# Kernel tuning notes

Hardware: AMD Instinct MI355X
Metric: run time of the kernel (lower is better)

The kernel has to match this reference:

```python
import jax, jax.numpy as jnp
import numpy as np

B, T, V, H, C = 512, 512, 64, 128, 4


def setup_inputs() -> dict:
    key = jax.random.key(0)
    ks = jax.random.split(key, 32)
    s = 0.05  # weight scale
    inp = {
        'x': jax.random.normal(ks[0], (B, T, V), jnp.float32),
        'd': jax.random.uniform(ks[1], (B, T, 1), jnp.float32),
        'm1': (jax.random.uniform(ks[2], (B, T, V)) < 0.5).astype(jnp.float32),
        'h0_1': 0.1 * jax.random.normal(ks[3], (B, H), jnp.float32),
        'h0_2': 0.1 * jax.random.normal(ks[4], (B, H), jnp.float32),
        'h0_3': 0.1 * jax.random.normal(ks[5], (B, H), jnp.float32),
        'W_ih1': s * jax.random.normal(ks[6], (3 * H, V), jnp.float32),
        'W_hh1': s * jax.random.normal(ks[7], (3 * H, H), jnp.float32),
        'b_ih1': jnp.zeros((3 * H,), jnp.float32),
        'b_hh1': jnp.zeros((3 * H,), jnp.float32),
        'W_ih2': s * jax.random.normal(ks[8], (3 * H, H), jnp.float32),
        'W_hh2': s * jax.random.normal(ks[9], (3 * H, H), jnp.float32),
        'b_ih2': jnp.zeros((3 * H,), jnp.float32),
        'b_hh2': jnp.zeros((3 * H,), jnp.float32),
        'W_ih3': s * jax.random.normal(ks[10], (3 * H, H), jnp.float32),
        'W_hh3': s * jax.random.normal(ks[11], (3 * H, H), jnp.float32),
        'b_ih3': jnp.zeros((3 * H,), jnp.float32),
        'b_hh3': jnp.zeros((3 * H,), jnp.float32),
        'W_out': s * jax.random.normal(ks[12], (C, H), jnp.float32),
        'b_out': jax.random.uniform(ks[13], (C,), jnp.float32),
        'W_dx': s * jax.random.normal(ks[14], (V, 1), jnp.float32),
        'b_dx': jax.random.uniform(ks[15], (V,), jnp.float32),
        'W_dh': s * jax.random.normal(ks[16], (H, 1), jnp.float32),
        'b_dh': jax.random.uniform(ks[17], (H,), jnp.float32),
    }
    return inp


def _gru_cell(xt, h, Wih, Whh, bih, bhh):
    # torch.nn.GRUCell math
    gi = xt @ Wih.T + bih          # [B, 3H]
    gh = h @ Whh.T + bhh           # [B, 3H]
    ir, iz, inn = jnp.split(gi, 3, axis=1)
    hr, hz, hn = jnp.split(gh, 3, axis=1)
    r = jax.nn.sigmoid(ir + hr)
    z = jax.nn.sigmoid(iz + hz)
    n = jnp.tanh(inn + r * hn)
    return (1.0 - z) * n + z * h


def reference(x, d, m1, h0_1, h0_2, h0_3,
              W_ih1, W_hh1, b_ih1, b_hh1,
              W_ih2, W_hh2, b_ih2, b_hh2,
              W_ih3, W_hh3, b_ih3, b_hh3,
              W_out, b_out, W_dx, b_dx, W_dh, b_dh):
    x0 = x[:, 0, :]  # first observation used for imputation

    def head(h):
        return jax.nn.softmax(h @ W_out.T + b_out, axis=1)

    # t = 0: no decay, raw input
    h1 = _gru_cell(x0, h0_1, W_ih1, W_hh1, b_ih1, b_hh1)
    h2 = _gru_cell(h1, h0_2, W_ih2, W_hh2, b_ih2, b_hh2)
    h3 = _gru_cell(h2, h0_3, W_ih3, W_hh3, b_ih3, b_hh3)
    y0 = head(h3)

    # time-major scan inputs for t = 1..T-1
    xs = (jnp.swapaxes(x[:, 1:, :], 0, 1),   # x_t
          jnp.swapaxes(x[:, :-1, :], 0, 1),  # x_{t-1}
          jnp.swapaxes(m1[:, 1:, :], 0, 1),  # m_t
          jnp.swapaxes(d[:, 1:, :], 0, 1))   # d_t [T-1, B, 1]

    def step(carry, inp):
        h1, h2, h3 = carry
        xt, xp, mt, dt = inp
        gamma_h = jnp.exp(-jax.nn.relu(dt @ W_dh.T + b_dh))  # [B, H]
        h1 = h1 * gamma_h
        h2 = h2 * gamma_h
        h3 = h3 * gamma_h
        gamma_x = jnp.exp(-jax.nn.relu(dt @ W_dx.T + b_dx))  # [B, V]
        x1 = (xp * gamma_x + (1.0 - gamma_x) * x0) * (1.0 - mt) + mt * xt
        h1 = _gru_cell(x1, h1, W_ih1, W_hh1, b_ih1, b_hh1)
        h2 = _gru_cell(h1, h2, W_ih2, W_hh2, b_ih2, b_hh2)
        h3 = _gru_cell(h2, h3, W_ih3, W_hh3, b_ih3, b_hh3)
        return (h1, h2, h3), head(h3)

    _, ys = jax.lax.scan(step, (h1, h2, h3), xs)  # [T-1, B, C]
    Y = jnp.concatenate([y0[None], ys], axis=0)    # [T, B, C]
    return jnp.swapaxes(Y, 0, 1)                   # [B, T, C]
```

## Files before the change

kernel.cpp:

```cpp
#include <hip/hip_runtime.h>

#define TT 512
#define VV 64
#define RING 16

typedef _Float16 f16;
typedef f16 f16x8 __attribute__((ext_vector_type(8)));
typedef f16 f16x4 __attribute__((ext_vector_type(4)));
typedef float f32x4v __attribute__((ext_vector_type(4)));
typedef unsigned long long u64;
typedef unsigned u32;

typedef __attribute__((address_space(1))) unsigned gu32;
typedef __attribute__((address_space(1))) unsigned long long gu64;

#define MFMA(A_,B_,C_) __builtin_amdgcn_mfma_f32_16x16x32_f16((A_),(B_),(C_),0,0,0)
#define AT_LD32(p)   __hip_atomic_load((gu32*)(void*)(p), __ATOMIC_RELAXED, __HIP_MEMORY_SCOPE_AGENT)
#define AT_ST32(p,v) __hip_atomic_store((gu32*)(void*)(p),(v), __ATOMIC_RELAXED, __HIP_MEMORY_SCOPE_AGENT)
#define AT_LD64(p)   __hip_atomic_load((gu64*)(void*)(p), __ATOMIC_RELAXED, __HIP_MEMORY_SCOPE_AGENT)
#define AT_ST64(p,v) __hip_atomic_store((gu64*)(void*)(p),(v), __ATOMIC_RELAXED, __HIP_MEMORY_SCOPE_AGENT)

__device__ __forceinline__ void barrier_lds(){ asm volatile("s_waitcnt lgkmcnt(0)\n\ts_barrier" ::: "memory"); }
__device__ __forceinline__ void wait_vm0(){ asm volatile("s_waitcnt vmcnt(0)" ::: "memory"); }
__device__ __forceinline__ float4 ld4(const float* p){ return *(const float4*)p; }

__device__ __forceinline__ f16x8 ldA8(const float* p){
  f16x8 a;
  #pragma unroll
  for (int j = 0; j < 8; ++j) a[j] = (f16)p[j];
  return a;
}

__device__ __forceinline__ int fragOff16(int d0, int b){
  const int kt = d0 >> 5, qq = (d0 >> 3) & 3, j0 = d0 & 7;
  return (kt*64 + qq*16 + b)*8 + j0;
}

__device__ __forceinline__ void fragW_lds(f16x8* buf, int d0, int b, const float* h4){
  f16x4 v;
  #pragma unroll
  for (int e = 0; e < 4; ++e) v[e] = (f16)h4[e];
  *(f16x4*)((f16*)buf + fragOff16(d0, b)) = v;
}

__device__ __forceinline__ void pubFrag(char* slot, int d0, int b, const float* h4){
  union { f16x4 v; u64 u; } uu;
  #pragma unroll
  for (int e = 0; e < 4; ++e) uu.v[e] = (f16)h4[e];
  AT_ST64((u64*)(slot + fragOff16(d0, b)*2), uu.u);
}

__device__ __forceinline__ f16x8 impFrag(const char* slot, int kt, int lane){
  union { u64 u[2]; f16x8 v; } vv;
  const u64* p = (const u64*)(slot + (kt*64 + lane)*16);
  vv.u[0] = AT_LD64((u64*)p);
  vv.u[1] = AT_LD64((u64*)(p + 1));
  return vv.v;
}

__device__ __forceinline__ void spin_ge(u32* f, u32 val){
  if ((threadIdx.x & 63) == 0){
    u32 g = 0;
    while (AT_LD32(f) < val && ++g < (1u << 20)) {}
  }
  asm volatile("" ::: "memory");
}

__device__ __forceinline__ void gates_upd2(const f32x4v& C0, const f32x4v& C1,
                                           const f32x4v& Ci2, const f32x4v& Ch2,
                                           const float* bR, const float* bZ,
                                           const float* bI, const float* bH,
                                           float* hp){
  #pragma unroll
  for (int e = 0; e < 4; ++e){
    float rr = 1.f/(1.f + __expf(-(C0[e] + bR[e])));
    float zz = 1.f/(1.f + __expf(-(C1[e] + bZ[e])));
    float nv = Ci2[e] + bI[e] + rr*(Ch2[e] + bH[e]);
    float nn = 1.f - 2.f/(1.f + __expf(2.f*nv));
    hp[e] = (1.f - zz)*nn + zz*hp[e];
  }
}

__global__ void k_init(u32* wsf){
  const int i = blockIdx.x*256 + threadIdx.x;
  if (i < 4096) AT_ST32(wsf + i, 0u);
}

__launch_bounds__(512, 1)
__global__ void k_pipe(const float* __restrict__ x,   const float* __restrict__ dd,
                       const float* __restrict__ m1,
                       const float* __restrict__ h01, const float* __restrict__ h02,
                       const float* __restrict__ h03,
                       const float* __restrict__ Wih1, const float* __restrict__ Whh1,
                       const float* __restrict__ bih1, const float* __restrict__ bhh1,
                       const float* __restrict__ Wih2, const float* __restrict__ Whh2,
                       const float* __restrict__ bih2, const float* __restrict__ bhh2,
                       const float* __restrict__ Wih3, const float* __restrict__ Whh3,
                       const float* __restrict__ bih3, const float* __restrict__ bhh3,
                       const float* __restrict__ Wout, const float* __restrict__ bout,
                       const float* __restrict__ Wdx,  const float* __restrict__ bdx,
                       const float* __restrict__ Wdh,  const float* __restrict__ bdh,
                       float* __restrict__ y, u32* __restrict__ wsf, char* __restrict__ wsd)
{
  __shared__ f16x8 sW[8*12*64];
  __shared__ f16x8 sFrag[2][256];
  __shared__ f16x8 sX1[2][128];
  __shared__ f16x8 sHead[2][256];

  const int tid = threadIdx.x, wid = tid >> 6, lane = tid & 63;
  const int q = lane >> 4, r = lane & 15;
  const int blk = blockIdx.x, role = blk >> 5, grp = blk & 31, b0 = grp << 4;

  u32* const FL  = wsf;
  u32* const ACK = wsf + 1024;
  u32* const fl0 = FL  + grp*16;
  u32* const ak0 = ACK + grp*16;
  u32* const fl1 = FL  + (32+grp)*16;
  u32* const ak1 = ACK + (32+grp)*16;
  char* const ring0 = wsd + (size_t)grp*RING*4096;
  char* const ring1 = wsd + (size_t)(32+grp)*RING*4096;

  const int dG = wid*16 + 4*q;
  const int wbase = wid*12;

  const float* bihX = (role == 0) ? bih1 : (role == 1) ? bih2 : bih3;
  const float* bhhX = (role == 0) ? bhh1 : (role == 1) ? bhh2 : bhh3;
  const float* h0X  = (role == 0) ? h01  : (role == 1) ? h02  : h03;

  float bR[4], bZ[4], bI[4], bH[4], hS[4], WdhL[4], bdhL[4];
  #pragma unroll
  for (int e = 0; e < 4; ++e){
    const int d = dG + e;
    bR[e] = bihX[d] + bhhX[d];
    bZ[e] = bihX[128+d] + bhhX[128+d];
    bI[e] = bihX[256+d];
    bH[e] = bhhX[256+d];
    WdhL[e] = Wdh[d]; bdhL[e] = bdh[d];
  }
  { float4 a = ld4(h0X + (size_t)(b0+r)*128 + dG); hS[0]=a.x; hS[1]=a.y; hS[2]=a.z; hS[3]=a.w; }
  float dhC = 0.f, dhN = dd[(size_t)(b0+r)*TT + 1];

  if (role == 0){
    f16x8 Ai[3][2];
    #pragma unroll
    for (int g = 0; g < 3; ++g){
      const int mrow = (g*8 + wid)*16 + r;
      #pragma unroll
      for (int kt = 0; kt < 2; ++kt) Ai[g][kt] = ldA8(Wih1 + mrow*64 + kt*32 + q*8);
      #pragma unroll
      for (int kt = 0; kt < 4; ++kt)
        sW[(wbase + g*4 + kt)*64 + lane] = ldA8(Whh1 + mrow*128 + kt*32 + q*8);
    }
    const int bx = (wid & 3)*4 + q, v0 = 4*r;
    float Wdx4[4] = {0,0,0,0}, bdx4[4] = {0,0,0,0};
    float4 xC = {0,0,0,0}, x0v = {0,0,0,0}, xN = {0,0,0,0}, mN = {0,0,0,0};
    float4 xP = {0,0,0,0}, mC = {0,0,0,0};
    float dxC = 0.f, dxN = 0.f;
    if (wid < 4){
      #pragma unroll
      for (int e = 0; e < 4; ++e){ Wdx4[e] = Wdx[v0+e]; bdx4[e] = bdx[v0+e]; }
      xC  = ld4(x + ((size_t)(b0+bx)*TT + 0)*VV + v0);
      x0v = xC;
      xN  = ld4(x  + ((size_t)(b0+bx)*TT + 1)*VV + v0);
      mN  = ld4(m1 + ((size_t)(b0+bx)*TT + 1)*VV + v0);
      dxN = dd[(size_t)(b0+bx)*TT + 1];
      xP = xC; mC = mN; dxC = dxN;
    }
    __syncthreads();

    for (int t = 0; t < TT; ++t){
      const int par = t & 1;
      if ((t & 3) == 0 && t >= 16) spin_ge(ak0, (u32)(t-13));
      if (wid < 4){
        float xi[4];
        if (t == 0){ xi[0]=xC.x; xi[1]=xC.y; xi[2]=xC.z; xi[3]=xC.w; }
        else {
          const float* xc = (const float*)&xC; const float* xp = (const float*)&xP;
          const float* x0e = (const float*)&x0v; const float* me = (const float*)&mC;
          #pragma unroll
          for (int e = 0; e < 4; ++e){
            float gx = __expf(-fmaxf(dxC*Wdx4[e] + bdx4[e], 0.f));
            xi[e] = (xp[e]*gx + (1.f-gx)*x0e[e])*(1.f-me[e]) + me[e]*xc[e];
          }
        }
        fragW_lds(&sX1[par][0], v0, bx, xi);
      }
      if (t >= 1){
        #pragma unroll
        for (int e = 0; e < 4; ++e)
          hS[e] *= __expf(-fmaxf(dhC*WdhL[e] + bdhL[e], 0.f));
      }
      fragW_lds(&sFrag[par][0], dG, r, hS);
      barrier_lds();
      f16x8 bx1[2], bh4[4];
      #pragma unroll
      for (int kt = 0; kt < 2; ++kt) bx1[kt] = sX1[par][kt*64 + lane];
      #pragma unroll
      for (int kt = 0; kt < 4; ++kt) bh4[kt] = sFrag[par][kt*64 + lane];
      f32x4v C0 = {0,0,0,0}, C1 = {0,0,0,0}, Ci2 = {0,0,0,0}, Ch2 = {0,0,0,0};
      #pragma unroll
      for (int kt = 0; kt < 4; ++kt) C0  = MFMA(sW[(wbase + 0*4 + kt)*64 + lane], bh4[kt], C0);
      #pragma unroll
      for (int kt = 0; kt < 4; ++kt) C1  = MFMA(sW[(wbase + 1*4 + kt)*64 + lane], bh4[kt], C1);
      #pragma unroll
      for (int kt = 0; kt < 4; ++kt) Ch2 = MFMA(sW[(wbase + 2*4 + kt)*64 + lane], bh4[kt], Ch2);
      #pragma unroll
      for (int kt = 0; kt < 2; ++kt) C0  = MFMA(Ai[0][kt], bx1[kt], C0);
      #pragma unroll
      for (int kt = 0; kt < 2; ++kt) C1  = MFMA(Ai[1][kt], bx1[kt], C1);
      #pragma unroll
      for (int kt = 0; kt < 2; ++kt) Ci2 = MFMA(Ai[2][kt], bx1[kt], Ci2);
      gates_upd2(C0, C1, Ci2, Ch2, bR, bZ, bI, bH, hS);
      pubFrag(ring0 + (size_t)(t & (RING-1))*4096, dG, r, hS);
      if ((t & 3) == 3){
        wait_vm0();
        barrier_lds();
        if (tid == 0) AT_ST32(fl0, (u32)(t+1));
      }
      dhC = dhN;
      const int tp = (t+2 < TT) ? (t+2) : (TT-1);
      dhN = dd[(size_t)(b0+r)*TT + tp];
      if (wid < 4){
        xP = xC; xC = xN; mC = mN; dxC = dxN;
        xN  = ld4(x  + ((size_t)(b0+bx)*TT + tp)*VV + v0);
        mN  = ld4(m1 + ((size_t)(b0+bx)*TT + tp)*VV + v0);
        dxN = dd[(size_t)(b0+bx)*TT + tp];
      }
    }
    return;
  }

  if (role == 1){
    f16x8 Ah[3][4];
    #pragma unroll
    for (int g = 0; g < 3; ++g){
      const int mrow = (g*8 + wid)*16 + r;
      #pragma unroll
      for (int kt = 0; kt < 4; ++kt){
        sW[(wbase + g*4 + kt)*64 + lane] = ldA8(Wih2 + mrow*128 + kt*32 + q*8);
        Ah[g][kt] = ldA8(Whh2 + mrow*128 + kt*32 + q*8);
      }
    }
    __syncthreads();

    spin_ge(fl0, 8u);
    f16x8 bi[4];
    #pragma unroll
    for (int kt = 0; kt < 4; ++kt) bi[kt] = impFrag(ring0, kt, lane);

    for (int t = 0; t < TT; ++t){
      const int par = t & 1;
      if ((t & 3) == 0 && t >= 16) spin_ge(ak1, (u32)(t-13));
      if (t >= 1){
        #pragma unroll
        for (int e = 0; e < 4; ++e)
          hS[e] *= __expf(-fmaxf(dhC*WdhL[e] + bdhL[e], 0.f));
      }
      fragW_lds(&sFrag[par][0], dG, r, hS);
      barrier_lds();
      if (tid == 0) AT_ST32(ak0, (u32)t);
      f16x8 bh4[4];
      #pragma unroll
      for (int kt = 0; kt < 4; ++kt) bh4[kt] = sFrag[par][kt*64 + lane];
      f32x4v C0 = {0,0,0,0}, C1 = {0,0,0,0}, Ci2 = {0,0,0,0}, Ch2 = {0,0,0,0};
      #pragma unroll
      for (int kt = 0; kt < 4; ++kt) C0  = MFMA(Ah[0][kt], bh4[kt], C0);
      #pragma unroll
      for (int kt = 0; kt < 4; ++kt) C1  = MFMA(Ah[1][kt], bh4[kt], C1);
      #pragma unroll
      for (int kt = 0; kt < 4; ++kt) Ch2 = MFMA(Ah[2][kt], bh4[kt], Ch2);
      #pragma unroll
      for (int kt = 0; kt < 4; ++kt) C0  = MFMA(sW[(wbase + 0*4 + kt)*64 + lane], bi[kt], C0);
      #pragma unroll
      for (int kt = 0; kt < 4; ++kt) C1  = MFMA(sW[(wbase + 1*4 + kt)*64 + lane], bi[kt], C1);
      #pragma unroll
      for (int kt = 0; kt < 4; ++kt) Ci2 = MFMA(sW[(wbase + 2*4 + kt)*64 + lane], bi[kt], Ci2);
      if (t + 1 < TT){
        const char* sIn = ring0 + (size_t)((t+1) & (RING-1))*4096;
        #pragma unroll
        for (int kt = 0; kt < 4; ++kt) bi[kt] = impFrag(sIn, kt, lane);
      }
      gates_upd2(C0, C1, Ci2, Ch2, bR, bZ, bI, bH, hS);
      pubFrag(ring1 + (size_t)(t & (RING-1))*4096, dG, r, hS);
      if ((t & 3) == 3){
        wait_vm0();
        barrier_lds();
        if (tid == 0) AT_ST32(fl1, (u32)(t+1));
        if (t < TT-1) spin_ge(fl0, (u32)(t+7 <= TT ? t+7 : TT));
      }
      dhC = dhN;
      const int tp = (t+2 < TT) ? (t+2) : (TT-1);
      dhN = dd[(size_t)(b0+r)*TT + tp];
    }
    return;
  }

  {
    f16x8 Ah[3][4];
    #pragma unroll
    for (int g = 0; g < 3; ++g){
      const int mrow = (g*8 + wid)*16 + r;
      #pragma unroll
      for (int kt = 0; kt < 4; ++kt){
        sW[(wbase + g*4 + kt)*64 + lane] = ldA8(Wih3 + mrow*128 + kt*32 + q*8);
        Ah[g][kt] = ldA8(Whh3 + mrow*128 + kt*32 + q*8);
      }
    }
    f16x8 aO[4]; float bo4[4] = {0,0,0,0};
    if (wid == 4){
      #pragma unroll
      for (int kt = 0; kt < 4; ++kt){
        f16x8 a;
        #pragma unroll
        for (int j = 0; j < 8; ++j)
          a[j] = (r < 4) ? (f16)Wout[r*128 + kt*32 + q*8 + j] : (f16)0.f;
        aO[kt] = a;
      }
      #pragma unroll
      for (int e = 0; e < 4; ++e) bo4[e] = bout[e];
    }
    __syncthreads();

    spin_ge(fl1, 8u);
    f16x8 bi[4];
    #pragma unroll
    for (int kt = 0; kt < 4; ++kt) bi[kt] = impFrag(ring1, kt, lane);

    for (int s = 0; s <= TT; ++s){
      const int par = s & 1;
      fragW_lds(&sHead[par][0], dG, r, hS);
      if (s < TT){
        if (s >= 1){
          #pragma unroll
          for (int e = 0; e < 4; ++e)
            hS[e] *= __expf(-fmaxf(dhC*WdhL[e] + bdhL[e], 0.f));
        }
        fragW_lds(&sFrag[par][0], dG, r, hS);
      }
      barrier_lds();
      if (s < TT && tid == 0) AT_ST32(ak1, (u32)s);
      if (s < TT){
        f16x8 bh4[4];
        #pragma unroll
        for (int kt = 0; kt < 4; ++kt) bh4[kt] = sFrag[par][kt*64 + lane];
        f32x4v C0 = {0,0,0,0}, C1 = {0,0,0,0}, Ci2 = {0,0,0,0}, Ch2 = {0,0,0,0};
        #pragma unroll
        for (int kt = 0; kt < 4; ++kt) C0  = MFMA(Ah[0][kt], bh4[kt], C0);
        #pragma unroll
        for (int kt = 0; kt < 4; ++kt) C1  = MFMA(Ah[1][kt], bh4[kt], C1);
        #pragma unroll
        for (int kt = 0; kt < 4; ++kt) Ch2 = MFMA(Ah[2][kt], bh4[kt], Ch2);
        #pragma unroll
        for (int kt = 0; kt < 4; ++kt) C0  = MFMA(sW[(wbase + 0*4 + kt)*64 + lane], bi[kt], C0);
        #pragma unroll
        for (int kt = 0; kt < 4; ++kt) C1  = MFMA(sW[(wbase + 1*4 + kt)*64 + lane], bi[kt], C1);
        #pragma unroll
        for (int kt = 0; kt < 4; ++kt) Ci2 = MFMA(sW[(wbase + 2*4 + kt)*64 + lane], bi[kt], Ci2);
        if (s + 1 < TT){
          const char* sIn = ring1 + (size_t)((s+1) & (RING-1))*4096;
          #pragma unroll
          for (int kt = 0; kt < 4; ++kt) bi[kt] = impFrag(sIn, kt, lane);
        }
        gates_upd2(C0, C1, Ci2, Ch2, bR, bZ, bI, bH, hS);
      }
      if (s >= 1 && wid == 4){
        f32x4v cl = {0.f,0.f,0.f,0.f};
        #pragma unroll
        for (int kt = 0; kt < 4; ++kt) cl = MFMA(aO[kt], sHead[par][kt*64 + lane], cl);
        if (lane < 16){
          float l0 = cl[0]+bo4[0], l1 = cl[1]+bo4[1], l2 = cl[2]+bo4[2], l3 = cl[3]+bo4[3];
          float mx = fmaxf(fmaxf(l0,l1), fmaxf(l2,l3));
          float e0 = __expf(l0-mx), e1 = __expf(l1-mx), e2 = __expf(l2-mx), e3 = __expf(l3-mx);
          float inv = 1.f/(e0+e1+e2+e3);
          float4 o; o.x = e0*inv; o.y = e1*inv; o.z = e2*inv; o.w = e3*inv;
          *(float4*)(y + ((size_t)(b0+lane)*TT + (s-1))*4) = o;
        }
      }
      if ((s & 3) == 3 && s < TT-1) spin_ge(fl1, (u32)(s+7 <= TT ? s+7 : TT));
      dhC = dhN;
      const int tp = (s+2 < TT) ? (s+2) : (TT-1);
      dhN = dd[(size_t)(b0+r)*TT + tp];
    }
  }
}

extern "C" void kernel_launch(void* const* d_in, const int* in_sizes, int n_in,
                              void* d_out, int out_size, void* d_ws, size_t ws_size,
                              hipStream_t stream) {
  (void)in_sizes; (void)n_in; (void)out_size; (void)ws_size;
  u32*  wsf = (u32*)d_ws;
  char* wsd = (char*)d_ws + 16384;
  k_init<<<dim3(16), dim3(256), 0, stream>>>(wsf);
  k_pipe<<<dim3(96), dim3(512), 0, stream>>>(
      (const float*)d_in[0],  (const float*)d_in[1],  (const float*)d_in[2],
      (const float*)d_in[3],  (const float*)d_in[4],  (const float*)d_in[5],
      (const float*)d_in[6],  (const float*)d_in[7],  (const float*)d_in[8],  (const float*)d_in[9],
      (const float*)d_in[10], (const float*)d_in[11], (const float*)d_in[12], (const float*)d_in[13],
      (const float*)d_in[14], (const float*)d_in[15], (const float*)d_in[16], (const float*)d_in[17],
      (const float*)d_in[18], (const float*)d_in[19],
      (const float*)d_in[20], (const float*)d_in[21],
      (const float*)d_in[22], (const float*)d_in[23],
      (float*)d_out, wsf, wsd);
}
```

Measured before the change: 1.266 ms.

## Process 32 batch rows per block with two MFMA halves, halving grid

Each workgroup now handles 32 batch rows instead of 16, running the per-step GRU matmuls twice (two 16-column halves) with the LDS-resident weights reused across both. The grid shrinks from 96 to 48 blocks, and ring slots double to 8 KB per step. The aim is to amortize weight loading, barriers and flag synchronisation over more work per block. The cost is roughly twice the serial per-step latency inside each block, and fewer CUs are in use.

New measurement: 2.016 ms. +59.3%, slower.

```diff
diff --git a/kernel.cpp b/kernel.cpp
--- a/kernel.cpp
+++ b/kernel.cpp
@@ -3,6 +3,8 @@
 #define TT 512
 #define VV 64
 #define RING 16
+#define NG 16
+#define SLOTB 8192
 
 typedef _Float16 f16;
 typedef f16 f16x8 __attribute__((ext_vector_type(8)));
@@ -103,22 +105,22 @@
                        float* __restrict__ y, u32* __restrict__ wsf, char* __restrict__ wsd)
 {
   __shared__ f16x8 sW[8*12*64];
-  __shared__ f16x8 sFrag[2][256];
-  __shared__ f16x8 sX1[2][128];
-  __shared__ f16x8 sHead[2][256];
+  __shared__ f16x8 sFrag[2][512];
+  __shared__ f16x8 sXH[2][256];
+  __shared__ f16x8 sHead[2][512];
 
   const int tid = threadIdx.x, wid = tid >> 6, lane = tid & 63;
   const int q = lane >> 4, r = lane & 15;
-  const int blk = blockIdx.x, role = blk >> 5, grp = blk & 31, b0 = grp << 4;
+  const int blk = blockIdx.x, role = blk >> 4, grp = blk & (NG-1), b0 = grp << 5;
 
   u32* const FL  = wsf;
   u32* const ACK = wsf + 1024;
   u32* const fl0 = FL  + grp*16;
   u32* const ak0 = ACK + grp*16;
-  u32* const fl1 = FL  + (32+grp)*16;
-  u32* const ak1 = ACK + (32+grp)*16;
-  char* const ring0 = wsd + (size_t)grp*RING*4096;
-  char* const ring1 = wsd + (size_t)(32+grp)*RING*4096;
+  u32* const fl1 = FL  + (NG+grp)*16;
+  u32* const ak1 = ACK + (NG+grp)*16;
+  char* const ring0 = wsd + (size_t)grp*RING*SLOTB;
+  char* const ring1 = wsd + (size_t)(NG+grp)*RING*SLOTB;
 
   const int dG = wid*16 + 4*q;
   const int wbase = wid*12;
@@ -127,7 +129,8 @@
   const float* bhhX = (role == 0) ? bhh1 : (role == 1) ? bhh2 : bhh3;
   const float* h0X  = (role == 0) ? h01  : (role == 1) ? h02  : h03;
 
-  float bR[4], bZ[4], bI[4], bH[4], hS[4], WdhL[4], bdhL[4];
+  float bR[4], bZ[4], bI[4], bH[4], WdhL[4], bdhL[4];
+  float hS[2][4];
   #pragma unroll
   for (int e = 0; e < 4; ++e){
     const int d = dG + e;
@@ -137,8 +140,14 @@
     bH[e] = bhhX[256+d];
     WdhL[e] = Wdh[d]; bdhL[e] = bdh[d];
   }
-  { float4 a = ld4(h0X + (size_t)(b0+r)*128 + dG); hS[0]=a.x; hS[1]=a.y; hS[2]=a.z; hS[3]=a.w; }
-  float dhC = 0.f, dhN = dd[(size_t)(b0+r)*TT + 1];
+  { float4 a = ld4(h0X + (size_t)(b0+r)*128 + dG);
+    hS[0][0]=a.x; hS[0][1]=a.y; hS[0][2]=a.z; hS[0][3]=a.w; }
+  { float4 a = ld4(h0X + (size_t)(b0+16+r)*128 + dG);
+    hS[1][0]=a.x; hS[1][1]=a.y; hS[1][2]=a.z; hS[1][3]=a.w; }
+  float dhC[2], dhN[2];
+  dhC[0] = dhC[1] = 0.f;
+  dhN[0] = dd[(size_t)(b0+r)*TT + 1];
+  dhN[1] = dd[(size_t)(b0+16+r)*TT + 1];
 
   if (role == 0){
     f16x8 Ai[3][2];
@@ -151,81 +160,83 @@
       for (int kt = 0; kt < 4; ++kt)
         sW[(wbase + g*4 + kt)*64 + lane] = ldA8(Whh1 + mrow*128 + kt*32 + q*8);
     }
-    const int bx = (wid & 3)*4 + q, v0 = 4*r;
-    float Wdx4[4] = {0,0,0,0}, bdx4[4] = {0,0,0,0};
-    float4 xC = {0,0,0,0}, x0v = {0,0,0,0}, xN = {0,0,0,0}, mN = {0,0,0,0};
-    float4 xP = {0,0,0,0}, mC = {0,0,0,0};
-    float dxC = 0.f, dxN = 0.f;
-    if (wid < 4){
-      #pragma unroll
-      for (int e = 0; e < 4; ++e){ Wdx4[e] = Wdx[v0+e]; bdx4[e] = bdx[v0+e]; }
-      xC  = ld4(x + ((size_t)(b0+bx)*TT + 0)*VV + v0);
-      x0v = xC;
-      xN  = ld4(x  + ((size_t)(b0+bx)*TT + 1)*VV + v0);
-      mN  = ld4(m1 + ((size_t)(b0+bx)*TT + 1)*VV + v0);
-      dxN = dd[(size_t)(b0+bx)*TT + 1];
-      xP = xC; mC = mN; dxC = dxN;
-    }
+    const int bx = wid*4 + q, v0 = 4*r;
+    const int xh = bx >> 4, xc = bx & 15;
+    float Wdx4[4], bdx4[4];
+    #pragma unroll
+    for (int e = 0; e < 4; ++e){ Wdx4[e] = Wdx[v0+e]; bdx4[e] = bdx[v0+e]; }
+    float4 xC = ld4(x + ((size_t)(b0+bx)*TT + 0)*VV + v0);
+    const float4 x0v = xC;
+    float4 xN = ld4(x  + ((size_t)(b0+bx)*TT + 1)*VV + v0);
+    float4 mN = ld4(m1 + ((size_t)(b0+bx)*TT + 1)*VV + v0);
+    float dxN = dd[(size_t)(b0+bx)*TT + 1];
+    float4 xP = xC, mC = mN; float dxC = dxN;
     __syncthreads();
 
     for (int t = 0; t < TT; ++t){
       const int par = t & 1;
       if ((t & 3) == 0 && t >= 16) spin_ge(ak0, (u32)(t-13));
-      if (wid < 4){
+      {
         float xi[4];
         if (t == 0){ xi[0]=xC.x; xi[1]=xC.y; xi[2]=xC.z; xi[3]=xC.w; }
         else {
-          const float* xc = (const float*)&xC; const float* xp = (const float*)&xP;
+          const float* xc_ = (const float*)&xC; const float* xp = (const float*)&xP;
           const float* x0e = (const float*)&x0v; const float* me = (const float*)&mC;
           #pragma unroll
           for (int e = 0; e < 4; ++e){
             float gx = __expf(-fmaxf(dxC*Wdx4[e] + bdx4[e], 0.f));
-            xi[e] = (xp[e]*gx + (1.f-gx)*x0e[e])*(1.f-me[e]) + me[e]*xc[e];
+            xi[e] = (xp[e]*gx + (1.f-gx)*x0e[e])*(1.f-me[e]) + me[e]*xc_[e];
           }
         }
-        fragW_lds(&sX1[par][0], v0, bx, xi);
+        fragW_lds(&sXH[par][xh*128], v0, xc, xi);
       }
       if (t >= 1){
         #pragma unroll
-        for (int e = 0; e < 4; ++e)
-          hS[e] *= __expf(-fmaxf(dhC*WdhL[e] + bdhL[e], 0.f));
-      }
-      fragW_lds(&sFrag[par][0], dG, r, hS);
+        for (int hh = 0; hh < 2; ++hh)
+          #pragma unroll
+          for (int e = 0; e < 4; ++e)
+            hS[hh][e] *= __expf(-fmaxf(dhC[hh]*WdhL[e] + bdhL[e], 0.f));
+      }
+      fragW_lds(&sFrag[par][0],   dG, r, hS[0]);
+      fragW_lds(&sFrag[par][256], dG, r, hS[1]);
       barrier_lds();
-      f16x8 bx1[2], bh4[4];
-      #pragma unroll
-      for (int kt = 0; kt < 2; ++kt) bx1[kt] = sX1[par][kt*64 + lane];
-      #pragma unroll
-      for (int kt = 0; kt < 4; ++kt) bh4[kt] = sFrag[par][kt*64 + lane];
-      f32x4v C0 = {0,0,0,0}, C1 = {0,0,0,0}, Ci2 = {0,0,0,0}, Ch2 = {0,0,0,0};
-      #pragma unroll
-      for (int kt = 0; kt < 4; ++kt) C0  = MFMA(sW[(wbase + 0*4 + kt)*64 + lane], bh4[kt], C0);
-      #pragma unroll
-      for (int kt = 0; kt < 4; ++kt) C1  = MFMA(sW[(wbase + 1*4 + kt)*64 + lane], bh4[kt], C1);
-      #pragma unroll
-      for (int kt = 0; kt < 4; ++kt) Ch2 = MFMA(sW[(wbase + 2*4 + kt)*64 + lane], bh4[kt], Ch2);
-      #pragma unroll
-      for (int kt = 0; kt < 2; ++kt) C0  = MFMA(Ai[0][kt], bx1[kt], C0);
-      #pragma unroll
-      for (int kt = 0; kt < 2; ++kt) C1  = MFMA(Ai[1][kt], bx1[kt], C1);
-      #pragma unroll
-      for (int kt = 0; kt < 2; ++kt) Ci2 = MFMA(Ai[2][kt], bx1[kt], Ci2);
-      gates_upd2(C0, C1, Ci2, Ch2, bR, bZ, bI, bH, hS);
-      pubFrag(ring0 + (size_t)(t & (RING-1))*4096, dG, r, hS);
+      char* sOut = ring0 + (size_t)(t & (RING-1))*SLOTB;
+      #pragma unroll
+      for (int hh = 0; hh < 2; ++hh){
+        f16x8 bx1[2], bh4[4];
+        #pragma unroll
+        for (int kt = 0; kt < 2; ++kt) bx1[kt] = sXH[par][hh*128 + kt*64 + lane];
+        #pragma unroll
+        for (int kt = 0; kt < 4; ++kt) bh4[kt] = sFrag[par][hh*256 + kt*64 + lane];
+        f32x4v C0 = {0,0,0,0}, C1 = {0,0,0,0}, Ci2 = {0,0,0,0}, Ch2 = {0,0,0,0};
+        #pragma unroll
+        for (int kt = 0; kt < 4; ++kt) C0  = MFMA(sW[(wbase + 0*4 + kt)*64 + lane], bh4[kt], C0);
+        #pragma unroll
+        for (int kt = 0; kt < 4; ++kt) C1  = MFMA(sW[(wbase + 1*4 + kt)*64 + lane], bh4[kt], C1);
+        #pragma unroll
+        for (int kt = 0; kt < 4; ++kt) Ch2 = MFMA(sW[(wbase + 2*4 + kt)*64 + lane], bh4[kt], Ch2);
+        #pragma unroll
+        for (int kt = 0; kt < 2; ++kt) C0  = MFMA(Ai[0][kt], bx1[kt], C0);
+        #pragma unroll
+        for (int kt = 0; kt < 2; ++kt) C1  = MFMA(Ai[1][kt], bx1[kt], C1);
+        #pragma unroll
+        for (int kt = 0; kt < 2; ++kt) Ci2 = MFMA(Ai[2][kt], bx1[kt], Ci2);
+        gates_upd2(C0, C1, Ci2, Ch2, bR, bZ, bI, bH, hS[hh]);
+        pubFrag(sOut + hh*4096, dG, r, hS[hh]);
+      }
       if ((t & 3) == 3){
         wait_vm0();
         barrier_lds();
         if (tid == 0) AT_ST32(fl0, (u32)(t+1));
       }
-      dhC = dhN;
+      dhC[0] = dhN[0]; dhC[1] = dhN[1];
       const int tp = (t+2 < TT) ? (t+2) : (TT-1);
-      dhN = dd[(size_t)(b0+r)*TT + tp];
-      if (wid < 4){
-        xP = xC; xC = xN; mC = mN; dxC = dxN;
-        xN  = ld4(x  + ((size_t)(b0+bx)*TT + tp)*VV + v0);
-        mN  = ld4(m1 + ((size_t)(b0+bx)*TT + tp)*VV + v0);
-        dxN = dd[(size_t)(b0+bx)*TT + tp];
-      }
+      dhN[0] = dd[(size_t)(b0+r)*TT + tp];
+      dhN[1] = dd[(size_t)(b0+16+r)*TT + tp];
+      xP = xC; xC = xN; mC = mN; dxC = dxN;
+      xN  = ld4(x  + ((size_t)(b0+bx)*TT + tp)*VV + v0);
+      mN  = ld4(m1 + ((size_t)(b0+bx)*TT + tp)*VV + v0);
+      dxN = dd[(size_t)(b0+bx)*TT + tp];
     }
     return;
   }
@@ -244,53 +255,63 @@
     __syncthreads();
 
     spin_ge(fl0, 8u);
-    f16x8 bi[4];
-    #pragma unroll
-    for (int kt = 0; kt < 4; ++kt) bi[kt] = impFrag(ring0, kt, lane);
+    f16x8 bi[2][4];
+    #pragma unroll
+    for (int kt = 0; kt < 4; ++kt) bi[0][kt] = impFrag(ring0, kt, lane);
+    #pragma unroll
+    for (int kt = 0; kt < 4; ++kt) bi[1][kt] = impFrag(ring0 + 4096, kt, lane);
 
     for (int t = 0; t < TT; ++t){
       const int par = t & 1;
       if ((t & 3) == 0 && t >= 16) spin_ge(ak1, (u32)(t-13));
       if (t >= 1){
         #pragma unroll
-        for (int e = 0; e < 4; ++e)
-          hS[e] *= __expf(-fmaxf(dhC*WdhL[e] + bdhL[e], 0.f));
-      }
-      fragW_lds(&sFrag[par][0], dG, r, hS);
+        for (int hh = 0; hh < 2; ++hh)
+          #pragma unroll
+          for (int e = 0; e < 4; ++e)
+            hS[hh][e] *= __expf(-fmaxf(dhC[hh]*WdhL[e] + bdhL[e], 0.f));
+      }
+      fragW_lds(&sFrag[par][0],   dG, r, hS[0]);
+      fragW_lds(&sFrag[par][256], dG, r, hS[1]);
       barrier_lds();
       if (tid == 0) AT_ST32(ak0, (u32)t);
-      f16x8 bh4[4];
-      #pragma unroll
-      for (int kt = 0; kt < 4; ++kt) bh4[kt] = sFrag[par][kt*64 + lane];
-      f32x4v C0 = {0,0,0,0}, C1 = {0,0,0,0}, Ci2 = {0,0,0,0}, Ch2 = {0,0,0,0};
-      #pragma unroll
-      for (int kt = 0; kt < 4; ++kt) C0  = MFMA(Ah[0][kt], bh4[kt], C0);
-      #pragma unroll
-      for (int kt = 0; kt < 4; ++kt) C1  = MFMA(Ah[1][kt], bh4[kt], C1);
-      #pragma unroll
-      for (int kt = 0; kt < 4; ++kt) Ch2 = MFMA(Ah[2][kt], bh4[kt], Ch2);
-      #pragma unroll
-      for (int kt = 0; kt < 4; ++kt) C0  = MFMA(sW[(wbase + 0*4 + kt)*64 + lane], bi[kt], C0);
-      #pragma unroll
-      for (int kt = 0; kt < 4; ++kt) C1  = MFMA(sW[(wbase + 1*4 + kt)*64 + lane], bi[kt], C1);
-      #pragma unroll
-      for (int kt = 0; kt < 4; ++kt) Ci2 = MFMA(sW[(wbase + 2*4 + kt)*64 + lane], bi[kt], Ci2);
-      if (t + 1 < TT){
-        const char* sIn = ring0 + (size_t)((t+1) & (RING-1))*4096;
-        #pragma unroll
-        for (int kt = 0; kt < 4; ++kt) bi[kt] = impFrag(sIn, kt, lane);
-      }
-      gates_upd2(C0, C1, Ci2, Ch2, bR, bZ, bI, bH, hS);
-      pubFrag(ring1 + (size_t)(t & (RING-1))*4096, dG, r, hS);
+      char* sOut = ring1 + (size_t)(t & (RING-1))*SLOTB;
+      #pragma unroll
+      for (int hh = 0; hh < 2; ++hh){
+        f16x8 bh4[4];
+        #pragma unroll
+        for (int kt = 0; kt < 4; ++kt) bh4[kt] = sFrag[par][hh*256 + kt*64 + lane];
+        f32x4v C0 = {0,0,0,0}, C1 = {0,0,0,0}, Ci2 = {0,0,0,0}, Ch2 = {0,0,0,0};
+        #pragma unroll
+        for (int kt = 0; kt < 4; ++kt) C0  = MFMA(Ah[0][kt], bh4[kt], C0);
+        #pragma unroll
+        for (int kt = 0; kt < 4; ++kt) C1  = MFMA(Ah[1][kt], bh4[kt], C1);
+        #pragma unroll
+        for (int kt = 0; kt < 4; ++kt) Ch2 = MFMA(Ah[2][kt], bh4[kt], Ch2);
+        #pragma unroll
+        for (int kt = 0; kt < 4; ++kt) C0  = MFMA(sW[(wbase + 0*4 + kt)*64 + lane], bi[hh][kt], C0);
+        #pragma unroll
+        for (int kt = 0; kt < 4; ++kt) C1  = MFMA(sW[(wbase + 1*4 + kt)*64 + lane], bi[hh][kt], C1);
+        #pragma unroll
+        for (int kt = 0; kt < 4; ++kt) Ci2 = MFMA(sW[(wbase + 2*4 + kt)*64 + lane], bi[hh][kt], Ci2);
+        if (t + 1 < TT){
+          const char* sIn = ring0 + (size_t)((t+1) & (RING-1))*SLOTB + hh*4096;
+          #pragma unroll
+          for (int kt = 0; kt < 4; ++kt) bi[hh][kt] = impFrag(sIn, kt, lane);
+        }
+        gates_upd2(C0, C1, Ci2, Ch2, bR, bZ, bI, bH, hS[hh]);
+        pubFrag(sOut + hh*4096, dG, r, hS[hh]);
+      }
       if ((t & 3) == 3){
         wait_vm0();
         barrier_lds();
         if (tid == 0) AT_ST32(fl1, (u32)(t+1));
         if (t < TT-1) spin_ge(fl0, (u32)(t+7 <= TT ? t+7 : TT));
       }
-      dhC = dhN;
+      dhC[0] = dhN[0]; dhC[1] = dhN[1];
       const int tp = (t+2 < TT) ? (t+2) : (TT-1);
-      dhN = dd[(size_t)(b0+r)*TT + tp];
+      dhN[0] = dd[(size_t)(b0+r)*TT + tp];
+      dhN[1] = dd[(size_t)(b0+16+r)*TT + tp];
     }
     return;
   }
@@ -307,7 +328,7 @@
       }
     }
     f16x8 aO[4]; float bo4[4] = {0,0,0,0};
-    if (wid == 4){
+    if (wid == 4 || wid == 5){
       #pragma unroll
       for (int kt = 0; kt < 4; ++kt){
         f16x8 a;
@@ -322,64 +343,75 @@
     __syncthreads();
 
     spin_ge(fl1, 8u);
-    f16x8 bi[4];
-    #pragma unroll
-    for (int kt = 0; kt < 4; ++kt) bi[kt] = impFrag(ring1, kt, lane);
+    f16x8 bi[2][4];
+    #pragma unroll
+    for (int kt = 0; kt < 4; ++kt) bi[0][kt] = impFrag(ring1, kt, lane);
+    #pragma unroll
+    for (int kt = 0; kt < 4; ++kt) bi[1][kt] = impFrag(ring1 + 4096, kt, lane);
 
     for (int s = 0; s <= TT; ++s){
       const int par = s & 1;
-      fragW_lds(&sHead[par][0], dG, r, hS);
+      fragW_lds(&sHead[par][0],   dG, r, hS[0]);
+      fragW_lds(&sHead[par][256], dG, r, hS[1]);
       if (s < TT){
         if (s >= 1){
           #pragma unroll
-          for (int e = 0; e < 4; ++e)
-            hS[e] *= __expf(-fmaxf(dhC*WdhL[e] + bdhL[e], 0.f));
+          for (int hh = 0; hh < 2; ++hh)
+            #pragma unroll
+            for (int e = 0; e < 4; ++e)
+              hS[hh][e] *= __expf(-fmaxf(dhC[hh]*WdhL[e] + bdhL[e], 0.f));
         }
-        fragW_lds(&sFrag[par][0], dG, r, hS);
+        fragW_lds(&sFrag[par][0],   dG, r, hS[0]);
+        fragW_lds(&sFrag[par][256], dG, r, hS[1]);
       }
       barrier_lds();
       if (s < TT && tid == 0) AT_ST32(ak1, (u32)s);
       if (s < TT){
-        f16x8 bh4[4];
-        #pragma unroll
-        for (int kt = 0; kt < 4; ++kt) bh4[kt] = sFrag[par][kt*64 + lane];
-        f32x4v C0 = {0,0,0,0}, C1 = {0,0,0,0}, Ci2 = {0,0,0,0}, Ch2 = {0,0,0,0};
-        #pragma unroll
-        for (int kt = 0; kt < 4; ++kt) C0  = MFMA(Ah[0][kt], bh4[kt], C0);
-        #pragma unroll
-        for (int kt = 0; kt < 4; ++kt) C1  = MFMA(Ah[1][kt], bh4[kt], C1);
-        #pragma unroll
-        for (int kt = 0; kt < 4; ++kt) Ch2 = MFMA(Ah[2][kt], bh4[kt], Ch2);
-        #pragma unroll
-        for (int kt = 0; kt < 4; ++kt) C0  = MFMA(sW[(wbase + 0*4 + kt)*64 + lane], bi[kt], C0);
-        #pragma unroll
-        for (int kt = 0; kt < 4; ++kt) C1  = MFMA(sW[(wbase + 1*4 + kt)*64 + lane], bi[kt], C1);
-        #pragma unroll
-        for (int kt = 0; kt < 4; ++kt) Ci2 = MFMA(sW[(wbase + 2*4 + kt)*64 + lane], bi[kt], Ci2);
-        if (s + 1 < TT){
-          const char* sIn = ring1 + (size_t)((s+1) & (RING-1))*4096;
-          #pragma unroll
-          for (int kt = 0; kt < 4; ++kt) bi[kt] = impFrag(sIn, kt, lane);
+        #pragma unroll
+        for (int hh = 0; hh < 2; ++hh){
+          f16x8 bh4[4];
+          #pragma unroll
+          for (int kt = 0; kt < 4; ++kt) bh4[kt] = sFrag[par][hh*256 + kt*64 + lane];
+          f32x4v C0 = {0,0,0,0}, C1 = {0,0,0,0}, Ci2 = {0,0,0,0}, Ch2 = {0,0,0,0};
+          #pragma unroll
+          for (int kt = 0; kt < 4; ++kt) C0  = MFMA(Ah[0][kt], bh4[kt], C0);
+          #pragma unroll
+          for (int kt = 0; kt < 4; ++kt) C1  = MFMA(Ah[1][kt], bh4[kt], C1);
+          #pragma unroll
+          for (int kt = 0; kt < 4; ++kt) Ch2 = MFMA(Ah[2][kt], bh4[kt], Ch2);
+          #pragma unroll
+          for (int kt = 0; kt < 4; ++kt) C0  = MFMA(sW[(wbase + 0*4 + kt)*64 + lane], bi[hh][kt], C0);
+          #pragma unroll
+          for (int kt = 0; kt < 4; ++kt) C1  = MFMA(sW[(wbase + 1*4 + kt)*64 + lane], bi[hh][kt], C1);
+          #pragma unroll
+          for (int kt = 0; kt < 4; ++kt) Ci2 = MFMA(sW[(wbase + 2*4 + kt)*64 + lane], bi[hh][kt], Ci2);
+          if (s + 1 < TT){
+            const char* sIn = ring1 + (size_t)((s+1) & (RING-1))*SLOTB + hh*4096;
+            #pragma unroll
+            for (int kt = 0; kt < 4; ++kt) bi[hh][kt] = impFrag(sIn, kt, lane);
+          }
+          gates_upd2(C0, C1, Ci2, Ch2, bR, bZ, bI, bH, hS[hh]);
         }
-        gates_upd2(C0, C1, Ci2, Ch2, bR, bZ, bI, bH, hS);
-      }
-      if (s >= 1 && wid == 4){
+      }
+      if (s >= 1 && (wid == 4 || wid == 5)){
+        const int hh = wid - 4;
         f32x4v cl = {0.f,0.f,0.f,0.f};
         #pragma unroll
-        for (int kt = 0; kt < 4; ++kt) cl = MFMA(aO[kt], sHead[par][kt*64 + lane], cl);
+        for (int kt = 0; kt < 4; ++kt) cl = MFMA(aO[kt], sHead[par][hh*256 + kt*64 + lane], cl);
         if (lane < 16){
           float l0 = cl[0]+bo4[0], l1 = cl[1]+bo4[1], l2 = cl[2]+bo4[2], l3 = cl[3]+bo4[3];
           float mx = fmaxf(fmaxf(l0,l1), fmaxf(l2,l3));
           float e0 = __expf(l0-mx), e1 = __expf(l1-mx), e2 = __expf(l2-mx), e3 = __expf(l3-mx);
           float inv = 1.f/(e0+e1+e2+e3);
           float4 o; o.x = e0*inv; o.y = e1*inv; o.z = e2*inv; o.w = e3*inv;
-          *(float4*)(y + ((size_t)(b0+lane)*TT + (s-1))*4) = o;
+          *(float4*)(y + ((size_t)(b0 + hh*16 + lane)*TT + (s-1))*4) = o;
         }
       }
       if ((s & 3) == 3 && s < TT-1) spin_ge(fl1, (u32)(s+7 <= TT ? s+7 : TT));
-      dhC = dhN;
+      dhC[0] = dhN[0]; dhC[1] = dhN[1];
       const int tp = (s+2 < TT) ? (s+2) : (TT-1);
-      dhN = dd[(size_t)(b0+r)*TT + tp];
+      dhN[0] = dd[(size_t)(b0+r)*TT + tp];
+      dhN[1] = dd[(size_t)(b0+16+r)*TT + tp];
     }
   }
 }
@@ -391,7 +423,7 @@
   u32*  wsf = (u32*)d_ws;
   char* wsd = (char*)d_ws + 16384;
   k_init<<<dim3(16), dim3(256), 0, stream>>>(wsf);
-  k_pipe<<<dim3(96), dim3(512), 0, stream>>>(
+  k_pipe<<<dim3(48), dim3(512), 0, stream>>>(
       (const float*)d_in[0],  (const float*)d_in[1],  (const float*)d_in[2],
       (const float*)d_in[3],  (const float*)d_in[4],  (const float*)d_in[5],
       (const float*)d_in[6],  (const float*)d_in[7],  (const float*)d_in[8],  (const float*)d_in[9],
```
